# Performance work log

Hardware: AMD Instinct MI355X
Metric: run time of the kernel (lower is better)

## Reference

```python
import jax, jax.numpy as jnp
import numpy as np

N_SUP, D = 4096, 128
N_CLASSES, SHOTS = 128, 32          # balanced episode: N_SUP = N_CLASSES * SHOTS
N_QUERY = 65536
N_BOOT = 8                          # num_bootstrap_samples


def setup_inputs() -> dict:
    key = jax.random.key(0)
    k_sup, k_q, k_boot = jax.random.split(key, 3)
    support_set_repr = jax.random.normal(k_sup, (N_SUP, D), dtype=jnp.float32)
    # balanced, sorted labels: class c owns contiguous block [c*SHOTS, (c+1)*SHOTS)
    support_labels = (jnp.arange(N_SUP, dtype=jnp.int32) // SHOTS).astype(jnp.int32)
    query_set_repr = jax.random.normal(k_q, (N_QUERY, D), dtype=jnp.float32)
    # externalized torch.randint(0, num_samples, (B, num_samples)) per class
    bootstrap_indices = jax.random.randint(
        k_boot, (N_BOOT, N_CLASSES, SHOTS), 0, SHOTS, dtype=jnp.int32)
    return {
        "support_set_repr": support_set_repr,
        "support_labels": support_labels,
        "query_set_repr": query_set_repr,
        "bootstrap_indices": bootstrap_indices,
    }


def reference(support_set_repr, support_labels, query_set_repr, bootstrap_indices):
    B, C, S = bootstrap_indices.shape
    d = support_set_repr.shape[-1]
    # labels are sorted & balanced (arange // SHOTS), so per-class gather == reshape
    class_repr = support_set_repr.reshape(C, S, d)              # [C, S, D]
    # fused bootstrap gather: [B, C, S, D]
    boot = jnp.take_along_axis(class_repr[None], bootstrap_indices[..., None], axis=2)
    protos = boot.mean(axis=2)                                   # [B, C, D]
    # cdist(q, protos, p=2) via ||q||^2 + ||p||^2 - 2 q.p
    q2 = jnp.sum(query_set_repr * query_set_repr, axis=-1)       # [NQ]
    p2 = jnp.sum(protos * protos, axis=-1)                       # [B, C]
    qp = jnp.einsum('qd,bcd->bqc', query_set_repr, protos)       # [B, NQ, C]
    d2 = q2[None, :, None] + p2[:, None, :] - 2.0 * qp
    dists = jnp.sqrt(jnp.maximum(d2, 0.0))                       # [B, NQ, C]
    # logits = mean over bootstraps of -dists
    return -dists.mean(axis=0)                                   # [NQ, C]
```

## Files before the change

kernel.cpp:

```cpp
#include <hip/hip_runtime.h>
#include <hip/hip_bf16.h>


#define DIM   128
#define NCLS  128
#define SHOTS 32
#define NB    8
#define NQ    65536

using short8 = __attribute__((ext_vector_type(8))) short;
using f32x4  = __attribute__((ext_vector_type(4))) float;

__device__ __forceinline__ unsigned short f2bf(float x) {
  union { float f; unsigned u; } v; v.f = x;
  unsigned r = v.u + 0x7fffu + ((v.u >> 16) & 1u);
  return (unsigned short)(r >> 16);
}

__device__ __forceinline__ short8 pack8_bf16(float4 a, float4 b) {
  __hip_bfloat162 p0 = __float22bfloat162_rn(make_float2(a.x, a.y));
  __hip_bfloat162 p1 = __float22bfloat162_rn(make_float2(a.z, a.w));
  __hip_bfloat162 p2 = __float22bfloat162_rn(make_float2(b.x, b.y));
  __hip_bfloat162 p3 = __float22bfloat162_rn(make_float2(b.z, b.w));
  union { __hip_bfloat162 h[4]; short8 s; } u;
  u.h[0] = p0; u.h[1] = p1; u.h[2] = p2; u.h[3] = p3;
  return u.s;
}

__device__ __forceinline__ float fast_sqrt(float x) {
#if __has_builtin(__builtin_amdgcn_sqrtf)
  return __builtin_amdgcn_sqrtf(x);
#else
  return sqrtf(x);
#endif
}

__global__ __launch_bounds__(128) void proto_kernel(
    const float* __restrict__ sup, const int* __restrict__ bidx,
    unsigned short* __restrict__ pfrag, float* __restrict__ p2) {
  int bc = blockIdx.x;
  int c  = bc & (NCLS - 1);
  int d  = threadIdx.x;
  __shared__ int   sidx[SHOTS];
  __shared__ float wsum[2];
  if (d < SHOTS) sidx[d] = bidx[bc * SHOTS + d];
  __syncthreads();
  float acc = 0.f;
  const float* base = sup + c * SHOTS * DIM + d;
  #pragma unroll
  for (int s = 0; s < SHOTS; ++s) acc += base[sidx[s] * DIM];
  float proto = acc * (1.0f / 32.0f);

  int b     = bc >> 7;
  int ct    = c >> 4, l15c = c & 15;
  int kiter = d >> 5, quad = (d >> 3) & 3, j = d & 7;
  int lane  = l15c + (quad << 4);
  int slot  = (b * 8 + ct) * 4 + kiter;
  pfrag[slot * 512 + lane * 8 + j] = f2bf(proto * -0.03125f);

  float sq = proto * proto;
  #pragma unroll
  for (int off = 32; off > 0; off >>= 1) sq += __shfl_down(sq, off, 64);
  if ((d & 63) == 0) wsum[d >> 6] = sq;
  __syncthreads();
  if (d == 0) p2[bc] = (wsum[0] + wsum[1]) * (1.0f / 64.0f);
}

#define SLOT_STRIDE 520

__global__ __launch_bounds__(256, 2) void dist_kernel(
    const float* __restrict__ q, const uint4* __restrict__ pfrag,
    const float* __restrict__ p2, float* __restrict__ out) {
  int tid  = threadIdx.x;
  int w    = tid >> 6, lane = tid & 63;
  int l15  = lane & 15, quad = lane >> 4;
  int q0   = blockIdx.x << 6;

  __shared__ unsigned short aflds[16 * SLOT_STRIDE];
  __shared__ float q2s[64];

  #pragma unroll
  for (int pass = 0; pass < 2; ++pass) {
    int rloc  = w * 16 + pass * 8 + (lane >> 3);
    int chunk = lane & 7;
    const float* src = q + (size_t)(q0 + rloc) * DIM + chunk * 16;
    float4 x0 = *reinterpret_cast<const float4*>(src);
    float4 x1 = *reinterpret_cast<const float4*>(src + 4);
    float4 x2 = *reinterpret_cast<const float4*>(src + 8);
    float4 x3 = *reinterpret_cast<const float4*>(src + 12);
    float s = x0.x*x0.x + x0.y*x0.y + x0.z*x0.z + x0.w*x0.w
            + x1.x*x1.x + x1.y*x1.y + x1.z*x1.z + x1.w*x1.w
            + x2.x*x2.x + x2.y*x2.y + x2.z*x2.z + x2.w*x2.w
            + x3.x*x3.x + x3.y*x3.y + x3.z*x3.z + x3.w*x3.w;
    s += __shfl_down(s, 4, 8);
    s += __shfl_down(s, 2, 8);
    s += __shfl_down(s, 1, 8);
    if (chunk == 0) q2s[rloc] = s;

    int mt = rloc >> 4, m = rloc & 15, i = chunk >> 1, h = chunk & 1;
    unsigned short* base = &aflds[(mt * 4 + i) * SLOT_STRIDE];
    *reinterpret_cast<short8*>(&base[((h * 2 + 0) * 16 + m) * 8]) = pack8_bf16(x0, x1);
    *reinterpret_cast<short8*>(&base[((h * 2 + 1) * 16 + m) * 8]) = pack8_bf16(x2, x3);
  }
  __syncthreads();

  short8 af[4][4];
  #pragma unroll
  for (int mt = 0; mt < 4; ++mt)
    #pragma unroll
    for (int k = 0; k < 4; ++k)
      af[mt][k] = *reinterpret_cast<const short8*>(
          &aflds[(mt * 4 + k) * SLOT_STRIDE + lane * 8]);

  f32x4 q2r[4];
  #pragma unroll
  for (int mt = 0; mt < 4; ++mt)
    #pragma unroll
    for (int r = 0; r < 4; ++r)
      q2r[mt][r] = q2s[mt * 16 + quad * 4 + r] * (1.0f / 64.0f);

  float p2v[NB][2];
  #pragma unroll
  for (int b = 0; b < NB; ++b)
    #pragma unroll
    for (int jj = 0; jj < 2; ++jj)
      p2v[b][jj] = p2[b * NCLS + (w * 2 + jj) * 16 + l15];

  f32x4 oacc[4][2];
  #pragma unroll
  for (int mt = 0; mt < 4; ++mt)
    #pragma unroll
    for (int jj = 0; jj < 2; ++jj)
      oacc[mt][jj] = (f32x4){0.f, 0.f, 0.f, 0.f};

  uint4 bufX[8], bufY[8];

  #define LOAD_B(BUF, B)                                                      \
    {                                                                         \
      _Pragma("unroll")                                                       \
      for (int jj = 0; jj < 2; ++jj) {                                        \
        int ct = w * 2 + jj;                                                  \
        const uint4* bp = pfrag + (size_t)(((B) * 8 + ct) * 4) * 64 + lane;   \
        _Pragma("unroll")                                                     \
        for (int k = 0; k < 4; ++k) BUF[jj * 4 + k] = bp[k * 64];             \
      }                                                                       \
    }

  #define COMPUTE_B(BUF, B)                                                   \
    {                                                                         \
      _Pragma("unroll")                                                       \
      for (int jj = 0; jj < 2; ++jj) {                                        \
        f32x4 qp[4];                                                          \
        _Pragma("unroll")                                                     \
        for (int mt = 0; mt < 4; ++mt)                                        \
          _Pragma("unroll")                                                   \
          for (int r = 0; r < 4; ++r)                                         \
            qp[mt][r] = q2r[mt][r] + p2v[B][jj];                              \
        _Pragma("unroll")                                                     \
        for (int k = 0; k < 4; ++k) {                                         \
          short8 bfk = __builtin_bit_cast(short8, BUF[jj * 4 + k]);           \
          _Pragma("unroll")                                                   \
          for (int mt = 0; mt < 4; ++mt)                                      \
            qp[mt] = __builtin_amdgcn_mfma_f32_16x16x32_bf16(af[mt][k], bfk, qp[mt], 0, 0, 0); \
        }                                                                     \
        _Pragma("unroll")                                                     \
        for (int mt = 0; mt < 4; ++mt)                                        \
          _Pragma("unroll")                                                   \
          for (int r = 0; r < 4; ++r)                                         \
            oacc[mt][jj][r] += fast_sqrt(fmaxf(qp[mt][r], 0.0f));             \
      }                                                                       \
    }

  LOAD_B(bufX, 0)
  #pragma unroll 1
  for (int i = 0; i < NB; i += 2) {
    LOAD_B(bufY, i + 1)
    COMPUTE_B(bufX, i)
    LOAD_B(bufX, (i + 2) & (NB - 1))
    COMPUTE_B(bufY, i + 1)
  }
  #undef LOAD_B
  #undef COMPUTE_B

  #pragma unroll
  for (int mt2 = 0; mt2 < 4; ++mt2)
    #pragma unroll
    for (int jj = 0; jj < 2; ++jj) {
      int col = (w * 2 + jj) * 16 + l15;
      #pragma unroll
      for (int r = 0; r < 4; ++r) {
        int row = q0 + mt2 * 16 + quad * 4 + r;
        out[(size_t)row * NCLS + col] = -oacc[mt2][jj][r];
      }
    }
}

extern "C" void kernel_launch(void* const* d_in, const int* in_sizes, int n_in,
                              void* d_out, int out_size, void* d_ws, size_t ws_size,
                              hipStream_t stream) {
  const float* sup   = (const float*)d_in[0];
  const float* query = (const float*)d_in[2];
  const int*   bidx  = (const int*)d_in[3];
  float* out = (float*)d_out;

  unsigned short* pfrag = (unsigned short*)d_ws;
  float* p2 = (float*)((char*)d_ws + (size_t)NB * NCLS * DIM * 2);

  proto_kernel<<<NB * NCLS, 128, 0, stream>>>(sup, bidx, pfrag, p2);
  dist_kernel<<<NQ / 64, 256, 0, stream>>>(query, (const uint4*)pfrag, p2, out);
}
```

Measured before the change: 110.8 us.

## Cut dist_kernel register pressure to raise occupancy to three blocks per CU

Raises the launch bound minimum from 2 to 3 blocks per SM and restructures the B-prefetch pipeline to move one class tile (4 uint4 loads plus one p2 scalar) per stage instead of two. This halves the prefetch buffers. Per-lane q2 and p2 register arrays are dropped in favour of LDS reads of q2 and on-the-fly p2 loads. The aim is to free VGPRs for more resident waves to hide latency. The cost is extra LDS and global reads inside the loop, and possible spills if the register cap is too tight.

```diff
diff --git a/kernel.cpp b/kernel.cpp
--- a/kernel.cpp
+++ b/kernel.cpp
@@ -68,7 +68,7 @@
 
 #define SLOT_STRIDE 520
 
-__global__ __launch_bounds__(256, 2) void dist_kernel(
+__global__ __launch_bounds__(256, 3) void dist_kernel(
     const float* __restrict__ q, const uint4* __restrict__ pfrag,
     const float* __restrict__ p2, float* __restrict__ out) {
   int tid  = threadIdx.x;
@@ -95,7 +95,7 @@
     s += __shfl_down(s, 4, 8);
     s += __shfl_down(s, 2, 8);
     s += __shfl_down(s, 1, 8);
-    if (chunk == 0) q2s[rloc] = s;
+    if (chunk == 0) q2s[rloc] = s * (1.0f / 64.0f);
 
     int mt = rloc >> 4, m = rloc & 15, i = chunk >> 1, h = chunk & 1;
     unsigned short* base = &aflds[(mt * 4 + i) * SLOT_STRIDE];
@@ -112,87 +112,72 @@
       af[mt][k] = *reinterpret_cast<const short8*>(
           &aflds[(mt * 4 + k) * SLOT_STRIDE + lane * 8]);
 
-  f32x4 q2r[4];
+  f32x4 oaccA[4], oaccB[4];
   #pragma unroll
-  for (int mt = 0; mt < 4; ++mt)
-    #pragma unroll
-    for (int r = 0; r < 4; ++r)
-      q2r[mt][r] = q2s[mt * 16 + quad * 4 + r] * (1.0f / 64.0f);
+  for (int mt = 0; mt < 4; ++mt) {
+    oaccA[mt] = (f32x4){0.f, 0.f, 0.f, 0.f};
+    oaccB[mt] = (f32x4){0.f, 0.f, 0.f, 0.f};
+  }
 
-  float p2v[NB][2];
-  #pragma unroll
-  for (int b = 0; b < NB; ++b)
-    #pragma unroll
-    for (int jj = 0; jj < 2; ++jj)
-      p2v[b][jj] = p2[b * NCLS + (w * 2 + jj) * 16 + l15];
+  const f32x4* q2v = reinterpret_cast<const f32x4*>(&q2s[quad * 4]);
 
-  f32x4 oacc[4][2];
-  #pragma unroll
-  for (int mt = 0; mt < 4; ++mt)
-    #pragma unroll
-    for (int jj = 0; jj < 2; ++jj)
-      oacc[mt][jj] = (f32x4){0.f, 0.f, 0.f, 0.f};
+  uint4 bufX[4], bufY[4];
+  float ppX, ppY;
 
-  uint4 bufX[8], bufY[8];
-
-  #define LOAD_B(BUF, B)                                                      \
+  #define LOAD_S(BUF, PP, B, JJ)                                              \
     {                                                                         \
+      const uint4* bp = pfrag + (size_t)((((B) * 8 + w * 2 + (JJ)) * 4)) * 64 + lane; \
       _Pragma("unroll")                                                       \
-      for (int jj = 0; jj < 2; ++jj) {                                        \
-        int ct = w * 2 + jj;                                                  \
-        const uint4* bp = pfrag + (size_t)(((B) * 8 + ct) * 4) * 64 + lane;   \
-        _Pragma("unroll")                                                     \
-        for (int k = 0; k < 4; ++k) BUF[jj * 4 + k] = bp[k * 64];             \
-      }                                                                       \
+      for (int k = 0; k < 4; ++k) BUF[k] = bp[k * 64];                        \
+      PP = p2[(B) * NCLS + (w * 2 + (JJ)) * 16 + l15];                        \
     }
 
-  #define COMPUTE_B(BUF, B)                                                   \
+  #define COMPUTE_S(BUF, PP, OA)                                              \
     {                                                                         \
+      f32x4 qp[4];                                                            \
       _Pragma("unroll")                                                       \
-      for (int jj = 0; jj < 2; ++jj) {                                        \
-        f32x4 qp[4];                                                          \
+      for (int mt = 0; mt < 4; ++mt) {                                        \
+        qp[mt] = q2v[mt * 4];                      \
+        _Pragma("unroll")                                                     \
+        for (int r = 0; r < 4; ++r) qp[mt][r] += PP;                          \
+      }                                                                       \
+      _Pragma("unroll")                                                       \
+      for (int k = 0; k < 4; ++k) {                                           \
+        short8 bfk = __builtin_bit_cast(short8, BUF[k]);                      \
         _Pragma("unroll")                                                     \
         for (int mt = 0; mt < 4; ++mt)                                        \
-          _Pragma("unroll")                                                   \
-          for (int r = 0; r < 4; ++r)                                         \
-            qp[mt][r] = q2r[mt][r] + p2v[B][jj];                              \
+          qp[mt] = __builtin_amdgcn_mfma_f32_16x16x32_bf16(af[mt][k], bfk, qp[mt], 0, 0, 0); \
+      }                                                                       \
+      _Pragma("unroll")                                                       \
+      for (int mt = 0; mt < 4; ++mt)                                          \
         _Pragma("unroll")                                                     \
-        for (int k = 0; k < 4; ++k) {                                         \
-          short8 bfk = __builtin_bit_cast(short8, BUF[jj * 4 + k]);           \
-          _Pragma("unroll")                                                   \
-          for (int mt = 0; mt < 4; ++mt)                                      \
-            qp[mt] = __builtin_amdgcn_mfma_f32_16x16x32_bf16(af[mt][k], bfk, qp[mt], 0, 0, 0); \
-        }                                                                     \
-        _Pragma("unroll")                                                     \
-        for (int mt = 0; mt < 4; ++mt)                                        \
-          _Pragma("unroll")                                                   \
-          for (int r = 0; r < 4; ++r)                                         \
-            oacc[mt][jj][r] += fast_sqrt(fmaxf(qp[mt][r], 0.0f));             \
-      }                                                                       \
+        for (int r = 0; r < 4; ++r)                                           \
+          OA[mt][r] += fast_sqrt(fmaxf(qp[mt][r], 0.0f));                     \
     }
 
-  LOAD_B(bufX, 0)
+  LOAD_S(bufX, ppX, 0, 0)
   #pragma unroll 1
-  for (int i = 0; i < NB; i += 2) {
-    LOAD_B(bufY, i + 1)
-    COMPUTE_B(bufX, i)
-    LOAD_B(bufX, (i + 2) & (NB - 1))
-    COMPUTE_B(bufY, i + 1)
+  for (int s = 0; s < 16; s += 2) {
+    int b = s >> 1;
+    LOAD_S(bufY, ppY, b, 1)
+    COMPUTE_S(bufX, ppX, oaccA)
+    LOAD_S(bufX, ppX, (b + 1) & (NB - 1), 0)
+    COMPUTE_S(bufY, ppY, oaccB)
   }
-  #undef LOAD_B
-  #undef COMPUTE_B
+  #undef LOAD_S
+  #undef COMPUTE_S
 
   #pragma unroll
-  for (int mt2 = 0; mt2 < 4; ++mt2)
+  for (int mt2 = 0; mt2 < 4; ++mt2) {
+    int colA = (w * 2 + 0) * 16 + l15;
+    int colB = (w * 2 + 1) * 16 + l15;
     #pragma unroll
-    for (int jj = 0; jj < 2; ++jj) {
-      int col = (w * 2 + jj) * 16 + l15;
-      #pragma unroll
-      for (int r = 0; r < 4; ++r) {
-        int row = q0 + mt2 * 16 + quad * 4 + r;
-        out[(size_t)row * NCLS + col] = -oacc[mt2][jj][r];
-      }
+    for (int r = 0; r < 4; ++r) {
+      int row = q0 + mt2 * 16 + quad * 4 + r;
+      out[(size_t)row * NCLS + colA] = -oaccA[mt2][r];
+      out[(size_t)row * NCLS + colB] = -oaccB[mt2][r];
     }
+  }
 }
 
 extern "C" void kernel_launch(void* const* d_in, const int* in_sizes, int n_in,
```

Measured after the change: 131.7 us. +18.9%, slower.
